# Kernel tuning notes

Measured on AMD Instinct MI355X. Metric: run time of the kernel, lower is better.

Reference implementation:

```python
import jax, jax.numpy as jnp
import numpy as np

B, V, N = 64, 64, 16384
R, Y = 32, 32          # obs_vocab, y_classes
HID = 128
BIG = 1.0e9


def _features(tables, sigma, base_obs, actions, responses, t):
    """Vectorized version of _score_one_step over the whole batch.

    tables: [B,V,N] int32 in [0,R); sigma: [B,N] int32 in [0,Y).
    Returns feat [B, V+1, 2] = stack([exp_amb, exp_sz], -1).
    """
    # candidate mask cand0 from base_obs and the (action, response) prefix
    m = tables[:, 0, :] == base_obs[:, None]                  # [B,N]
    used = jnp.zeros((B, V), dtype=bool)
    for i in range(t):
        a = actions[:, i]
        is_stop = a == V
        ac = jnp.clip(a, 0, V - 1)
        lbl = jnp.take_along_axis(tables, ac[:, None, None], axis=1)[:, 0, :]  # [B,N]
        m = m & (is_stop[:, None] | (lbl == responses[:, i][:, None]))
        used = used.at[jnp.arange(B), ac].max(~is_stop)
    mf = m.astype(jnp.float32)
    total0 = mf.sum(-1)                                       # [B]
    safe_tot = jnp.maximum(total0, 1.0)

    # per-(batch, action, response) bucket counts: counts[b,a,r] = |{n : cand0 & tables[b,a,n]==r}|
    b_ix = jnp.arange(B)[:, None, None]
    a_ix = jnp.arange(V)[None, :, None]
    flat = (b_ix * V + a_ix) * R + tables                     # [B,V,N]
    w = jnp.broadcast_to(mf[:, None, :], (B, V, N)).ravel()
    counts = jnp.zeros((B * V * R,), jnp.float32).at[flat.ravel()].add(w).reshape(B, V, R)

    # per-bucket distinct sigma values: presence[b,a,r,y] = 1 if some candidate in bucket has sigma==y
    flat2 = flat * Y + sigma[:, None, :]                      # [B,V,N]
    pres = jnp.zeros((B * V * R * Y,), jnp.float32).at[flat2.ravel()].max(w).reshape(B, V, R, Y)
    uniq = pres.sum(-1)                                       # [B,V,R]

    # expected size / ambiguity: sum_r (sz_r/total0)*sz_r and (sz_r/total0)*uniq_r
    exp_sz = (counts * counts).sum(-1) / safe_tot[:, None]    # [B,V]
    exp_amb = (counts * uniq).sum(-1) / safe_tot[:, None]     # [B,V]

    # forbid view 0 (forbid_view0=True in logits_query) and already-used actions
    forbidden = used.at[:, 0].set(True)
    exp_sz = jnp.where(forbidden, BIG, exp_sz)
    exp_amb = jnp.where(forbidden, BIG, exp_amb)

    # STOP action: ambiguity of cand0 itself, size = |cand0|
    pres0 = jnp.zeros((B * Y,), jnp.float32).at[(jnp.arange(B)[:, None] * Y + sigma).ravel()].max(mf.ravel()).reshape(B, Y)
    stop_amb = pres0.sum(-1)                                  # [B]

    amb_full = jnp.concatenate([exp_amb, stop_amb[:, None]], axis=1)   # [B,V+1]
    sz_full = jnp.concatenate([exp_sz, total0[:, None]], axis=1)       # [B,V+1]

    # empty candidate set -> all-zero features (torch early-return)
    empty = (total0 == 0.0)[:, None]
    amb_full = jnp.where(empty, 0.0, amb_full)
    sz_full = jnp.where(empty, 0.0, sz_full)
    return jnp.stack([amb_full, sz_full], axis=-1)            # [B,V+1,2]


def setup_inputs() -> dict:
    key = jax.random.key(0)
    ks = jax.random.split(key, 9)
    T = 8
    return {
        "tables": jax.random.randint(ks[0], (B, V, N), 0, R, dtype=jnp.int32),
        "sigma": jax.random.randint(ks[1], (B, N), 0, Y, dtype=jnp.int32),
        "base_obs": jax.random.randint(ks[2], (B,), 0, R, dtype=jnp.int32),
        "actions": jax.random.randint(ks[3], (B, T), 0, V + 1, dtype=jnp.int32),
        "responses": jax.random.randint(ks[4], (B, T), 0, R, dtype=jnp.int32),
        "W1": jax.random.normal(ks[5], (2, HID), jnp.float32) / np.sqrt(2.0).astype(np.float32),
        "b1": jax.random.normal(ks[6], (HID,), jnp.float32) * 0.01,
        "W2": jax.random.normal(ks[7], (HID, 1), jnp.float32) / np.sqrt(float(HID)).astype(np.float32),
        "b2": jax.random.normal(ks[8], (1,), jnp.float32) * 0.01,
        "t": 2,
        "max_steps": 8,
    }


def reference(tables, sigma, base_obs, actions, responses, W1, b1, W2, b2, t, max_steps):
    feat = _features(tables, sigma, base_obs, actions, responses, int(t))  # [B,V+1,2]
    h = jax.nn.gelu(feat @ W1 + b1, approximate=False)        # exact (erf) GELU like nn.GELU
    return (h @ W2 + b2)[..., 0]                              # [B, V+1] action logits
```

## Files before the change

### kernel.cpp

```cpp
#include <hip/hip_runtime.h>
#include <math.h>

#define B 64
#define V 64
#define NN 16384
#define RR 32
#define HIDN 128
#define BIGV 1000000000.0f
#define CAP 4096

__global__ __launch_bounds__(512)
void k_fused(const int* __restrict__ tables,
             const int* __restrict__ sigma,
             const int* __restrict__ base_obs,
             const int* __restrict__ actions,
             const int* __restrict__ responses,
             const int* __restrict__ t_ptr,
             const float* __restrict__ W1,
             const float* __restrict__ b1,
             const float* __restrict__ W2,
             const float* __restrict__ b2,
             float* __restrict__ out,
             int T)
{
    const int b = blockIdx.x;
    const int tid = threadIdx.x;

    __shared__ int s_cnt;
    __shared__ int s_list[CAP];
    __shared__ unsigned s_counts[RR * V];
    __shared__ unsigned s_mask[RR * V];
    __shared__ float s_feat[(V + 1) * 2];

    if (tid == 0) s_cnt = 0;
    for (int i = tid; i < RR * V; i += 512) { s_counts[i] = 0u; s_mask[i] = 0u; }
    __syncthreads();

    const int t = t_ptr[0];
    const int base = base_obs[b];
    const int* row0 = tables + (size_t)b * V * NN;

    for (int n0 = tid * 4; n0 < NN; n0 += 512 * 4) {
        const int4 tv = *(const int4*)(row0 + n0);
        int m0 = (tv.x == base), m1 = (tv.y == base), m2 = (tv.z == base), m3 = (tv.w == base);
        for (int i = 0; i < t; ++i) {
            const int a = actions[b * T + i];
            if (a == V) continue;
            const int resp = responses[b * T + i];
            const int4 lv = *(const int4*)(row0 + a * NN + n0);
            m0 &= (lv.x == resp); m1 &= (lv.y == resp); m2 &= (lv.z == resp); m3 &= (lv.w == resp);
        }
        if (m0) { int i = atomicAdd(&s_cnt, 1); if (i < CAP) s_list[i] = n0; }
        if (m1) { int i = atomicAdd(&s_cnt, 1); if (i < CAP) s_list[i] = n0 + 1; }
        if (m2) { int i = atomicAdd(&s_cnt, 1); if (i < CAP) s_list[i] = n0 + 2; }
        if (m3) { int i = atomicAdd(&s_cnt, 1); if (i < CAP) s_list[i] = n0 + 3; }
    }
    __syncthreads();

    const int K = min(s_cnt, CAP);
    const int* bsig = sigma + (size_t)b * NN;

    if (tid < V) {
        const int v = tid;
        const int* rowv = row0 + v * NN;
        for (int k = 0; k < K; ++k) {
            const int n = s_list[k];
            const int r = rowv[n];
            const int y = bsig[n];
            s_counts[r * V + v] += 1u;
            s_mask[r * V + v] |= (1u << y);
        }
    }
    __syncthreads();

    if (tid < V) {
        const int v = tid;
        const float safe = (K > 0) ? (float)K : 1.0f;
        float sz = 0.f, amb = 0.f;
        unsigned pm = 0u;
        for (int r = 0; r < RR; ++r) {
            const unsigned mk = s_mask[r * V + v];
            const float c = (float)s_counts[r * V + v];
            pm |= mk;
            sz += c * c;
            amb += c * (float)__popc(mk);
        }
        sz /= safe; amb /= safe;
        bool forb = (v == 0);
        for (int i = 0; i < t; ++i)
            if (actions[b * T + i] == v) forb = true;
        if (forb) { sz = BIGV; amb = BIGV; }
        s_feat[v * 2 + 0] = amb;
        s_feat[v * 2 + 1] = sz;
        if (v == 0) {
            s_feat[V * 2 + 0] = (float)__popc(pm);
            s_feat[V * 2 + 1] = (float)K;
        }
    }
    __syncthreads();

    if (tid <= V) {
        float f0 = 0.f, f1 = 0.f;
        if (K > 0) { f0 = s_feat[tid * 2 + 0]; f1 = s_feat[tid * 2 + 1]; }
        float acc = b2[0];
        for (int j = 0; j < HIDN; ++j) {
            const float x = f0 * W1[j] + f1 * W1[HIDN + j] + b1[j];
            const float g = 0.5f * x * (1.0f + erff(x * 0.70710678118654752f));
            acc = fmaf(g, W2[j], acc);
        }
        out[b * (V + 1) + tid] = acc;
    }
}

extern "C" void kernel_launch(void* const* d_in, const int* in_sizes, int n_in,
                              void* d_out, int out_size, void* d_ws, size_t ws_size,
                              hipStream_t stream) {
    const int* tables    = (const int*)d_in[0];
    const int* sigma     = (const int*)d_in[1];
    const int* base_obs  = (const int*)d_in[2];
    const int* actions   = (const int*)d_in[3];
    const int* responses = (const int*)d_in[4];
    const float* W1      = (const float*)d_in[5];
    const float* b1      = (const float*)d_in[6];
    const float* W2      = (const float*)d_in[7];
    const float* b2      = (const float*)d_in[8];
    const int* t_ptr     = (const int*)d_in[9];
    float* out = (float*)d_out;

    const int T = in_sizes[3] / B;

    k_fused<<<B, 512, 0, stream>>>(tables, sigma, base_obs, actions, responses,
                                   t_ptr, W1, b1, W2, b2, out, T);
}
```

Measured before the change: 348.0 us.

## Spread candidate histogram across all waves with LDS atomics, remove list cap

```diff
diff --git a/kernel.cpp b/kernel.cpp
--- a/kernel.cpp
+++ b/kernel.cpp
@@ -7,9 +7,10 @@
 #define RR 32
 #define HIDN 128
 #define BIGV 1000000000.0f
-#define CAP 4096
+#define NTHR 1024
+#define NWAVE (NTHR / 64)
 
-__global__ __launch_bounds__(512)
+__global__ __launch_bounds__(NTHR)
 void k_fused(const int* __restrict__ tables,
              const int* __restrict__ sigma,
              const int* __restrict__ base_obs,
@@ -27,20 +28,20 @@
     const int tid = threadIdx.x;
 
     __shared__ int s_cnt;
-    __shared__ int s_list[CAP];
+    __shared__ int s_list[NN];
     __shared__ unsigned s_counts[RR * V];
     __shared__ unsigned s_mask[RR * V];
     __shared__ float s_feat[(V + 1) * 2];
 
     if (tid == 0) s_cnt = 0;
-    for (int i = tid; i < RR * V; i += 512) { s_counts[i] = 0u; s_mask[i] = 0u; }
+    for (int i = tid; i < RR * V; i += NTHR) { s_counts[i] = 0u; s_mask[i] = 0u; }
     __syncthreads();
 
     const int t = t_ptr[0];
     const int base = base_obs[b];
     const int* row0 = tables + (size_t)b * V * NN;
 
-    for (int n0 = tid * 4; n0 < NN; n0 += 512 * 4) {
+    for (int n0 = tid * 4; n0 < NN; n0 += NTHR * 4) {
         const int4 tv = *(const int4*)(row0 + n0);
         int m0 = (tv.x == base), m1 = (tv.y == base), m2 = (tv.z == base), m3 = (tv.w == base);
         for (int i = 0; i < t; ++i) {
@@ -50,25 +51,27 @@
             const int4 lv = *(const int4*)(row0 + a * NN + n0);
             m0 &= (lv.x == resp); m1 &= (lv.y == resp); m2 &= (lv.z == resp); m3 &= (lv.w == resp);
         }
-        if (m0) { int i = atomicAdd(&s_cnt, 1); if (i < CAP) s_list[i] = n0; }
-        if (m1) { int i = atomicAdd(&s_cnt, 1); if (i < CAP) s_list[i] = n0 + 1; }
-        if (m2) { int i = atomicAdd(&s_cnt, 1); if (i < CAP) s_list[i] = n0 + 2; }
-        if (m3) { int i = atomicAdd(&s_cnt, 1); if (i < CAP) s_list[i] = n0 + 3; }
+        if (m0) { int i = atomicAdd(&s_cnt, 1); s_list[i] = n0; }
+        if (m1) { int i = atomicAdd(&s_cnt, 1); s_list[i] = n0 + 1; }
+        if (m2) { int i = atomicAdd(&s_cnt, 1); s_list[i] = n0 + 2; }
+        if (m3) { int i = atomicAdd(&s_cnt, 1); s_list[i] = n0 + 3; }
     }
     __syncthreads();
 
-    const int K = min(s_cnt, CAP);
+    const int K = s_cnt;
     const int* bsig = sigma + (size_t)b * NN;
 
-    if (tid < V) {
-        const int v = tid;
+    {
+        const int v = tid & 63;
+        const int w = tid >> 6;
         const int* rowv = row0 + v * NN;
-        for (int k = 0; k < K; ++k) {
+        #pragma unroll 4
+        for (int k = w; k < K; k += NWAVE) {
             const int n = s_list[k];
             const int r = rowv[n];
             const int y = bsig[n];
-            s_counts[r * V + v] += 1u;
-            s_mask[r * V + v] |= (1u << y);
+            atomicAdd(&s_counts[r * V + v], 1u);
+            atomicOr(&s_mask[r * V + v], 1u << y);
         }
     }
     __syncthreads();
@@ -129,6 +132,6 @@
 
     const int T = in_sizes[3] / B;
 
-    k_fused<<<B, 512, 0, stream>>>(tables, sigma, base_obs, actions, responses,
-                                   t_ptr, W1, b1, W2, b2, out, T);
+    k_fused<<<B, NTHR, 0, stream>>>(tables, sigma, base_obs, actions, responses,
+                                    t_ptr, W1, b1, W2, b2, out, T);
 }
```

Result: no change. 342.2 us (-1.6%).
